# Performance work log

Measured on AMD Instinct MI355X. Metric: run time of the kernel, lower is better.

Reference implementation:

```python
import jax, jax.numpy as jnp
import numpy as np

B, N, DIM, H = 16, 1024, 512, 8
HEAD_DIM = DIM // H
SCALE = HEAD_DIM ** -0.5


def _dct_matrix(m):
    # Orthonormal DCT-II matrix, matching cv2.dct: D[0,:]=sqrt(1/m),
    # D[k,n]=sqrt(2/m)*cos(pi*(2n+1)*k/(2m)) for k>0.
    n = jnp.arange(m, dtype=jnp.float32)
    k = n[:, None]
    D = jnp.sqrt(2.0 / m) * jnp.cos(jnp.pi * (2.0 * n[None, :] + 1.0) * k / (2.0 * m))
    return D.at[0, :].set(jnp.sqrt(1.0 / m))


def setup_inputs() -> dict:
    key = jax.random.key(0)
    ks = jax.random.split(key, 9)
    def lin(k, fan_in, shape):
        return jax.random.normal(k, shape, jnp.float32) * (1.0 / np.sqrt(fan_in))
    return {
        "x": jax.random.normal(ks[0], (B, N, DIM), jnp.float32),
        "qkv_w": lin(ks[1], DIM, (DIM, 3 * DIM)),
        "qkv_b": lin(ks[2], DIM, (3 * DIM,)),
        "proj_w": lin(ks[3], DIM, (DIM, DIM)),
        "proj_b": lin(ks[4], DIM, (DIM,)),
        "h1_w": lin(ks[5], DIM, (DIM, DIM // 4)),
        "h1_b": jnp.zeros((DIM // 4,), jnp.float32),
        "h2_w": lin(ks[6], DIM // 4, (DIM // 4, H)),
        "h2_b": jnp.zeros((H,), jnp.float32),
        "freq_w": jnp.float32(0.5),
    }


def _extract_dct_features(x):
    # x: (B, N, C). Mirrors extract_dct_features incl. the .detach() in torch.
    B_, N_, _ = x.shape
    m = int(np.ceil(np.sqrt(N_)))  # static
    x_mean = x.mean(axis=-1)                                   # (B, N)
    A = jnp.pad(x_mean, ((0, 0), (0, m * m - N_))).reshape(B_, m, m)
    D = _dct_matrix(m)
    dct2 = jnp.einsum('km,bmn,ln->bkl', D, A, D)               # 2D DCT per sample
    dct_feat = dct2.reshape(B_, m * m)[:, :N_]
    dct_feat = jnp.clip(dct_feat, -10.0, 10.0)
    norm = jnp.linalg.norm(dct_feat, axis=1, keepdims=True) + 1e-5
    return jax.lax.stop_gradient(dct_feat / norm)              # (B, N)


def reference(x, qkv_w, qkv_b, proj_w, proj_b, h1_w, h1_b, h2_w, h2_b, freq_w):
    B_, N_, C = x.shape
    # QKV projection -> (3, B, H, N, head_dim)
    qkv = (x @ qkv_w + qkv_b).reshape(B_, N_, 3, H, C // H)
    qkv = jnp.transpose(qkv, (2, 0, 3, 1, 4))
    q, k, v = qkv[0] * SCALE, qkv[1], qkv[2]
    attn = jnp.einsum('bhnd,bhmd->bhnm', q, k)                 # (B, H, N, N)

    # Frequency-domain attention term
    dct_feat = _extract_dct_features(x)                        # (B, N)
    x_avg = x.mean(axis=1)                                     # (B, C)
    head_w = jax.nn.relu(x_avg @ h1_w + h1_b) @ h2_w + h2_b    # (B, H)
    weighted = dct_feat[:, None, :] * head_w[:, :, None]       # (B, H, N)
    freq_attn = jnp.einsum('bhn,bhm->bnm', weighted, weighted) # (B, N, N)
    row_sum = jnp.maximum(freq_attn.sum(axis=-1, keepdims=True), 1e-5)
    freq_attn = jnp.clip(freq_attn / row_sum, 0.0, 1.0)

    aw = jax.nn.sigmoid(freq_w)
    attn = (1.0 - aw) * attn + aw * freq_attn[:, None, :, :]
    attn = jax.nn.softmax(attn, axis=-1)

    out = jnp.einsum('bhnm,bhmd->bhnd', attn, v)
    out = jnp.transpose(out, (0, 2, 1, 3)).reshape(B_, N_, C)
    return out @ proj_w + proj_b
```

## Files before the change

### kernel.cpp

```cpp
#include <hip/hip_runtime.h>
#include <hip/hip_bf16.h>
#include <math.h>

#define PI_F  3.14159265358979323846f
#define LOG2E 1.44269504088896340736f

typedef __attribute__((ext_vector_type(8))) short          bf16x8;
typedef __attribute__((ext_vector_type(8))) unsigned short ushort8;
typedef __attribute__((ext_vector_type(4))) float          f32x4;

__device__ __forceinline__ unsigned short f2bf(float f) {
  union { float f; unsigned u; } v; v.f = f;
  unsigned r = v.u + 0x7fffu + ((v.u >> 16) & 1u);
  return (unsigned short)(r >> 16);
}

__device__ __forceinline__ unsigned short f2bf_hw(float f) {
  __hip_bfloat16 h = __float2bfloat16(f);
  return *reinterpret_cast<unsigned short*>(&h);
}

#define GLOAD16(g, l)                                                         \
  __builtin_amdgcn_global_load_lds(                                           \
      (const __attribute__((address_space(1))) void*)(g),                     \
      (__attribute__((address_space(3))) void*)(l), 16, 0, 0)

static const size_t OFF_XB  = 0;
static const size_t OFF_QB  = 16777216;
static const size_t OFF_KB  = 33554432;
static const size_t OFF_VT  = 67108864;
static const size_t OFF_AO  = 83886080;
static const size_t OFF_WT  = 100663296;
static const size_t OFF_PWT = 102236160;
static const size_t OFF_XM  = 102760448;
static const size_t OFF_XA  = 102825984;
static const size_t OFF_DF  = 102858752;
static const size_t OFF_TS  = 102924288;
static const size_t OFF_CR  = 102924352;

__global__ __launch_bounds__(256) void k_xmean_cvt(const float* __restrict__ x,
                                                   float* __restrict__ xmean,
                                                   unsigned short* __restrict__ xb) {
  int row  = blockIdx.x * 4 + (threadIdx.x >> 6);
  int lane = threadIdx.x & 63;
  const float* px = x + (size_t)row * 512 + lane * 8;
  float4 a = ((const float4*)px)[0];
  float4 b = ((const float4*)px)[1];
  ushort8 o;
  o[0] = f2bf(a.x); o[1] = f2bf(a.y); o[2] = f2bf(a.z); o[3] = f2bf(a.w);
  o[4] = f2bf(b.x); o[5] = f2bf(b.y); o[6] = f2bf(b.z); o[7] = f2bf(b.w);
  *(ushort8*)(xb + (size_t)row * 512 + lane * 8) = o;
  float s = a.x + a.y + a.z + a.w + b.x + b.y + b.z + b.w;
  for (int off = 32; off; off >>= 1) s += __shfl_down(s, off);
  if (lane == 0) xmean[row] = s * (1.f / 512.f);
}

__global__ __launch_bounds__(512) void k_xavg(const unsigned short* __restrict__ xb,
                                              float* __restrict__ xavg) {
  int b = blockIdx.x, chunk = blockIdx.y;
  int c = threadIdx.x;
  const unsigned short* px = xb + ((size_t)b * 1024 + (size_t)chunk * 64) * 512 + c;
  float s = 0.f;
#pragma unroll 8
  for (int n = 0; n < 64; ++n) {
    unsigned u = (unsigned)px[(size_t)n * 512] << 16;
    s += *reinterpret_cast<float*>(&u);
  }
  atomicAdd(&xavg[b * 512 + c], s);
}

__global__ __launch_bounds__(1024) void k_dct(const float* __restrict__ xmean,
                                              float* __restrict__ dfeat,
                                              float* __restrict__ tsum) {
  __shared__ float A[32][33], Dm[32][33], Tm[32][33];
  __shared__ float red[1024];
  __shared__ float nrm;
  int b = blockIdx.x, t = threadIdx.x;
  int kk = t >> 5, nn = t & 31;
  A[kk][nn] = xmean[b * 1024 + t];
  float dv = (kk == 0) ? sqrtf(1.f / 32.f)
                       : sqrtf(2.f / 32.f) * cosf(PI_F * (2.f * nn + 1.f) * (float)kk / 64.f);
  Dm[kk][nn] = dv;
  __syncthreads();
  float acc = 0.f;
  for (int m = 0; m < 32; ++m) acc += Dm[kk][m] * A[m][nn];
  Tm[kk][nn] = acc;
  __syncthreads();
  float acc2 = 0.f;
  for (int n = 0; n < 32; ++n) acc2 += Tm[kk][n] * Dm[nn][n];
  float val = fminf(fmaxf(acc2, -10.f), 10.f);
  red[t] = val * val;
  __syncthreads();
  for (int s = 512; s; s >>= 1) { if (t < s) red[t] += red[t + s]; __syncthreads(); }
  if (t == 0) nrm = sqrtf(red[0]) + 1e-5f;
  __syncthreads();
  float dn = val / nrm;
  dfeat[b * 1024 + t] = dn;
  red[t] = dn;
  __syncthreads();
  for (int s = 512; s; s >>= 1) { if (t < s) red[t] += red[t + s]; __syncthreads(); }
  if (t == 0) tsum[b] = red[0];
}

__global__ __launch_bounds__(128) void k_headw(const float* __restrict__ xavg,
                                               const float* __restrict__ h1w,
                                               const float* __restrict__ h1b,
                                               const float* __restrict__ h2w,
                                               const float* __restrict__ h2b,
                                               const float* __restrict__ dfeat,
                                               const float* __restrict__ tsum,
                                               const float* __restrict__ freqw,
                                               float* __restrict__ crow) {
  __shared__ float xa[512];
  __shared__ float h1s[128];
  __shared__ float hw[8];
  int b = blockIdx.x, t = threadIdx.x;
  for (int i = t; i < 512; i += 128) xa[i] = xavg[b * 512 + i] * (1.f / 1024.f);
  __syncthreads();
  float acc = h1b[t];
  for (int c = 0; c < 512; ++c) acc += xa[c] * h1w[c * 128 + t];
  h1s[t] = fmaxf(acc, 0.f);
  __syncthreads();
  if (t < 8) {
    float a2 = h2b[t];
    for (int j = 0; j < 128; ++j) a2 += h1s[j] * h2w[j * 8 + t];
    hw[t] = a2;
  }
  __syncthreads();
  float s = 0.f;
#pragma unroll
  for (int h = 0; h < 8; ++h) s += hw[h] * hw[h];
  float Tb = tsum[b];
  const float aw2 = (1.f / (1.f + __expf(-freqw[0]))) * LOG2E;
  for (int n = t; n < 1024; n += 128) {
    float dn = dfeat[b * 1024 + n];
    float p = s * dn;
    crow[b * 1024 + n] = aw2 * p / fmaxf(p * Tb, 1e-5f);
  }
}

__global__ __launch_bounds__(256) void k_wtrans(const float* __restrict__ w,
                                                unsigned short* __restrict__ wt,
                                                int Nw) {
  __shared__ unsigned short T[64 * 65];
  int n0 = blockIdx.x * 64, k0 = blockIdx.y * 64;
  int t = threadIdx.x;
  int r = t >> 2, c0 = (t & 3) * 16;
  const float* src = w + (size_t)(k0 + r) * Nw + n0 + c0;
#pragma unroll
  for (int q = 0; q < 4; ++q) {
    float4 v4 = *(const float4*)(src + q * 4);
    T[(c0 + q * 4 + 0) * 65 + r] = f2bf(v4.x);
    T[(c0 + q * 4 + 1) * 65 + r] = f2bf(v4.y);
    T[(c0 + q * 4 + 2) * 65 + r] = f2bf(v4.z);
    T[(c0 + q * 4 + 3) * 65 + r] = f2bf(v4.w);
  }
  __syncthreads();
  int nl = t >> 2, koff = (t & 3) * 16;
  ushort8 o0, o1;
#pragma unroll
  for (int e = 0; e < 8; ++e) o0[e] = T[nl * 65 + koff + e];
#pragma unroll
  for (int e = 0; e < 8; ++e) o1[e] = T[nl * 65 + koff + 8 + e];
  unsigned short* dst = wt + (size_t)(n0 + nl) * 512 + k0 + koff;
  *(ushort8*)(dst) = o0;
  *(ushort8*)(dst + 8) = o1;
}

template <int MODE>
__global__ __launch_bounds__(256) void k_gemm(const unsigned short* __restrict__ A,
                                              const unsigned short* __restrict__ Bt,
                                              const float* __restrict__ bias,
                                              const float* __restrict__ freqw,
                                              unsigned short* __restrict__ o_q,
                                              unsigned short* __restrict__ o_k,
                                              unsigned short* __restrict__ o_vt,
                                              float* __restrict__ o_f) {
  __shared__ __align__(16) unsigned short As[128 * 64];
  __shared__ __align__(16) unsigned short Bs[128 * 64];
  const int t = threadIdx.x, w = t >> 6, l = t & 63;
  const int lg = l >> 4, ln = l & 15;
  const int wm = w >> 1, wn = w & 1;
  constexpr int NX = (MODE == 0) ? 12 : 4;
  const int bid = blockIdx.x, xcd = bid & 7, idx = bid >> 3;
  const int bx = idx % NX, by = xcd * 16 + idx / NX;
  const int row0 = by * 128, col0 = bx * 128;

  f32x4 acc[4][4];
#pragma unroll
  for (int i = 0; i < 4; ++i)
#pragma unroll
    for (int j = 0; j < 4; ++j) acc[i][j] = (f32x4){0.f, 0.f, 0.f, 0.f};

  int aoff[4][2], boff[4][2];
#pragma unroll
  for (int mt = 0; mt < 4; ++mt)
#pragma unroll
    for (int ks = 0; ks < 2; ++ks) {
      int ra = wm * 64 + mt * 16 + ln;
      aoff[mt][ks] = ra * 64 + (((lg + ks * 4) ^ (ra & 7)) << 3);
      int rb = wn * 64 + mt * 16 + ln;
      boff[mt][ks] = rb * 64 + (((lg + ks * 4) ^ (rb & 7)) << 3);
    }

  for (int k0 = 0; k0 < 512; k0 += 64) {
#pragma unroll
    for (int j = 0; j < 4; ++j) {
      int g = (j * 4 + w) * 64 + l;
      int row = g >> 3, slot = g & 7;
      int ss = slot ^ (row & 7);
      GLOAD16(A + (size_t)(row0 + row) * 512 + k0 + ss * 8, As + (size_t)(j * 4 + w) * 512);
      GLOAD16(Bt + (size_t)(col0 + row) * 512 + k0 + ss * 8, Bs + (size_t)(j * 4 + w) * 512);
    }
    __syncthreads();
#pragma unroll
    for (int ks = 0; ks < 2; ++ks) {
      bf16x8 av[4], bv[4];
#pragma unroll
      for (int mt = 0; mt < 4; ++mt) av[mt] = *(const bf16x8*)(As + aoff[mt][ks]);
#pragma unroll
      for (int nt = 0; nt < 4; ++nt) bv[nt] = *(const bf16x8*)(Bs + boff[nt][ks]);
#pragma unroll
      for (int mt = 0; mt < 4; ++mt)
#pragma unroll
        for (int nt = 0; nt < 4; ++nt)
          acc[mt][nt] = __builtin_amdgcn_mfma_f32_16x16x32_bf16(av[mt], bv[nt], acc[mt][nt], 0, 0, 0);
    }
    __syncthreads();
  }

  if (MODE == 0) {
    const int sel = col0 >> 9;
    if (sel == 2) {
      unsigned short* T = (wn == 0) ? As : Bs;
#pragma unroll
      for (int nt = 0; nt < 4; ++nt) {
        int dcol = nt * 16 + ln;
        float bcol = bias[col0 + wn * 64 + dcol];
#pragma unroll
        for (int mt = 0; mt < 4; ++mt)
#pragma unroll
          for (int r = 0; r < 4; ++r) {
            int rowL = wm * 64 + mt * 16 + lg * 4 + r;
            int slot = (rowL >> 3) ^ (dcol & 7);
            T[dcol * 128 + slot * 8 + (rowL & 7)] = f2bf(acc[mt][nt][r] + bcol);
          }
      }
      __syncthreads();
      int b_ = row0 >> 10, n0 = row0 & 1023;
      int h0 = (col0 & 511) >> 6;
      int dcol = t >> 2, rseg = (t & 3) * 32;
#pragma unroll
      for (int half = 0; half < 2; ++half) {
        const unsigned short* S = half ? Bs : As;
        size_t plane = ((size_t)(b_ * 8 + h0 + half)) << 16;
        unsigned short* dst = o_vt + plane + (size_t)dcol * 1024 + n0 + rseg;
#pragma unroll
        for (int j = 0; j < 4; ++j) {
          int slot = ((rseg >> 3) + j) ^ (dcol & 7);
          *(ushort8*)(dst + j * 8) = *(const ushort8*)(S + dcol * 128 + slot * 8);
        }
      }
      return;
    }
    unsigned short* outp = (sel == 0) ? o_q : o_k;
    const float aw = 1.f / (1.f + __expf(-freqw[0]));
    const float scl = (sel == 0) ? 0.125f * (1.f - aw) * LOG2E : 1.f;
#pragma unroll
    for (int nt = 0; nt < 4; ++nt) {
      int colg = col0 + wn * 64 + nt * 16 + ln;
      float bcol = bias[colg];
      int h = (colg >> 6) & 7, d = colg & 63;
#pragma unroll
      for (int mt = 0; mt < 4; ++mt)
#pragma unroll
        for (int r = 0; r < 4; ++r) {
          int row = row0 + wm * 64 + mt * 16 + lg * 4 + r;
          int bidx = row >> 10, n = row & 1023;
          float val = (acc[mt][nt][r] + bcol) * scl;
          outp[(((size_t)(bidx * 8 + h)) << 16) + (n << 6) + d] = f2bf(val);
        }
    }
  } else {
#pragma unroll
    for (int nt = 0; nt < 4; ++nt) {
      int colg = col0 + wn * 64 + nt * 16 + ln;
      float bcol = bias[colg];
#pragma unroll
      for (int mt = 0; mt < 4; ++mt)
#pragma unroll
        for (int r = 0; r < 4; ++r) {
          int row = row0 + wm * 64 + mt * 16 + lg * 4 + r;
          o_f[(size_t)row * 512 + colg] = acc[mt][nt][r] + bcol;
        }
    }
  }
}

__global__ __launch_bounds__(256) void k_attn(const unsigned short* __restrict__ qb,
                                              const unsigned short* __restrict__ kb,
                                              const unsigned short* __restrict__ vtg,
                                              const float* __restrict__ crow,
                                              const float* __restrict__ dfeat,
                                              const float* __restrict__ freqw,
                                              unsigned short* __restrict__ ao) {
  __shared__ __align__(16) unsigned short Ks[64 * 64];
  __shared__ __align__(16) unsigned short Vs[64 * 64];
  __shared__ __align__(16) unsigned short Ps[4][32 * 64];
  const int bid = blockIdx.x, xcd = bid & 7, idx = bid >> 3;
  const int bh = xcd * 16 + (idx >> 3), qt = idx & 7;
  const int b = bh >> 3, h = bh & 7;
  const int t = threadIdx.x, w = t >> 6, l = t & 63;
  const int lg = l >> 4, ln = l & 15;
  const size_t base = ((size_t)(b * 8 + h)) << 16;
  const float aw2 = (1.f / (1.f + __expf(-freqw[0]))) * LOG2E;

  const int qrow0 = qt * 128 + w * 32;
  bf16x8 qf[2][2];
#pragma unroll
  for (int mt = 0; mt < 2; ++mt)
#pragma unroll
    for (int ks = 0; ks < 2; ++ks)
      qf[mt][ks] = *(const bf16x8*)(qb + base + (size_t)(qrow0 + mt * 16 + ln) * 64 + lg * 8 + ks * 32);

  float cr2[2][4];
#pragma unroll
  for (int mt = 0; mt < 2; ++mt)
#pragma unroll
    for (int r = 0; r < 4; ++r)
      cr2[mt][r] = crow[b * 1024 + qrow0 + mt * 16 + lg * 4 + r];

  f32x4 accO[2][4];
#pragma unroll
  for (int mt = 0; mt < 2; ++mt)
#pragma unroll
    for (int dt = 0; dt < 4; ++dt) accO[mt][dt] = (f32x4){0.f, 0.f, 0.f, 0.f};
  float mrow[2][4], psum[2][4];
#pragma unroll
  for (int mt = 0; mt < 2; ++mt)
#pragma unroll
    for (int r = 0; r < 4; ++r) { mrow[mt][r] = -1e30f; psum[mt][r] = 0.f; }

  int rdoff[2];
#pragma unroll
  for (int ks = 0; ks < 2; ++ks) rdoff[ks] = ln * 64 + (((lg + ks * 4) ^ (ln & 7)) << 3);
  int pwoff[4][4];
#pragma unroll
  for (int nt = 0; nt < 4; ++nt)
#pragma unroll
    for (int r = 0; r < 4; ++r) {
      int prow = lg * 4 + r;
      pwoff[nt][r] = prow * 64 + ((((nt << 1) | (ln >> 3)) ^ (prow & 7)) << 3) + (ln & 7);
    }

  for (int kt = 0; kt < 16; ++kt) {
    __syncthreads();
#pragma unroll
    for (int j = 0; j < 2; ++j) {
      int g = (j * 4 + w) * 64 + l;
      int row = g >> 3, slot = g & 7;
      int ss = slot ^ (row & 7);
      GLOAD16(kb + base + (size_t)(kt * 64 + row) * 64 + ss * 8, Ks + (size_t)(j * 4 + w) * 512);
      GLOAD16(vtg + base + (size_t)row * 1024 + kt * 64 + ss * 8, Vs + (size_t)(j * 4 + w) * 512);
    }
    __syncthreads();

    float dmv[4];
#pragma unroll
    for (int nt = 0; nt < 4; ++nt) dmv[nt] = dfeat[b * 1024 + kt * 64 + nt * 16 + ln];
    f32x4 s[2][4];
#pragma unroll
    for (int mt = 0; mt < 2; ++mt)
#pragma unroll
      for (int nt = 0; nt < 4; ++nt)
#pragma unroll
        for (int r = 0; r < 4; ++r)
          s[mt][nt][r] = fminf(fmaxf(cr2[mt][r] * dmv[nt], 0.f), aw2);
#pragma unroll
    for (int nt = 0; nt < 4; ++nt) {
      bf16x8 kf0 = *(const bf16x8*)(Ks + nt * 1024 + rdoff[0]);
      bf16x8 kf1 = *(const bf16x8*)(Ks + nt * 1024 + rdoff[1]);
#pragma unroll
      for (int mt = 0; mt < 2; ++mt) {
        s[mt][nt] = __builtin_amdgcn_mfma_f32_16x16x32_bf16(qf[mt][0], kf0, s[mt][nt], 0, 0, 0);
        s[mt][nt] = __builtin_amdgcn_mfma_f32_16x16x32_bf16(qf[mt][1], kf1, s[mt][nt], 0, 0, 0);
      }
    }

    float lmax[2][4];
    bool viol = false;
#pragma unroll
    for (int mt = 0; mt < 2; ++mt)
#pragma unroll
      for (int r = 0; r < 4; ++r) {
        lmax[mt][r] = fmaxf(fmaxf(s[mt][0][r], s[mt][1][r]), fmaxf(s[mt][2][r], s[mt][3][r]));
        viol = viol || (lmax[mt][r] > mrow[mt][r] + 8.f);
      }
    if (__any(viol)) {
#pragma unroll
      for (int mt = 0; mt < 2; ++mt)
#pragma unroll
        for (int r = 0; r < 4; ++r) {
          float pmax = lmax[mt][r];
          pmax = fmaxf(pmax, __shfl_xor(pmax, 1));
          pmax = fmaxf(pmax, __shfl_xor(pmax, 2));
          pmax = fmaxf(pmax, __shfl_xor(pmax, 4));
          pmax = fmaxf(pmax, __shfl_xor(pmax, 8));
          float mnew = fmaxf(mrow[mt][r], pmax);
          float sc = exp2f(mrow[mt][r] - mnew);
          psum[mt][r] *= sc;
          mrow[mt][r] = mnew;
#pragma unroll
          for (int dt = 0; dt < 4; ++dt) accO[mt][dt][r] *= sc;
        }
    }
#pragma unroll
    for (int mt = 0; mt < 2; ++mt)
#pragma unroll
      for (int r = 0; r < 4; ++r) {
        float p0 = exp2f(s[mt][0][r] - mrow[mt][r]);
        float p1 = exp2f(s[mt][1][r] - mrow[mt][r]);
        float p2 = exp2f(s[mt][2][r] - mrow[mt][r]);
        float p3 = exp2f(s[mt][3][r] - mrow[mt][r]);
        psum[mt][r] += (p0 + p1) + (p2 + p3);
        Ps[w][mt * 1024 + pwoff[0][r]] = f2bf_hw(p0);
        Ps[w][mt * 1024 + pwoff[1][r]] = f2bf_hw(p1);
        Ps[w][mt * 1024 + pwoff[2][r]] = f2bf_hw(p2);
        Ps[w][mt * 1024 + pwoff[3][r]] = f2bf_hw(p3);
      }

    bf16x8 pa[2][2];
#pragma unroll
    for (int mt = 0; mt < 2; ++mt)
#pragma unroll
      for (int ks = 0; ks < 2; ++ks)
        pa[mt][ks] = *(const bf16x8*)(Ps[w] + mt * 1024 + rdoff[ks]);
#pragma unroll
    for (int dt = 0; dt < 4; ++dt) {
      bf16x8 vf0 = *(const bf16x8*)(Vs + dt * 1024 + rdoff[0]);
      bf16x8 vf1 = *(const bf16x8*)(Vs + dt * 1024 + rdoff[1]);
#pragma unroll
      for (int mt = 0; mt < 2; ++mt) {
        accO[mt][dt] = __builtin_amdgcn_mfma_f32_16x16x32_bf16(pa[mt][0], vf0, accO[mt][dt], 0, 0, 0);
        accO[mt][dt] = __builtin_amdgcn_mfma_f32_16x16x32_bf16(pa[mt][1], vf1, accO[mt][dt], 0, 0, 0);
      }
    }
  }

#pragma unroll
  for (int mt = 0; mt < 2; ++mt)
#pragma unroll
    for (int r = 0; r < 4; ++r) {
      float lr = psum[mt][r];
      lr += __shfl_xor(lr, 1);
      lr += __shfl_xor(lr, 2);
      lr += __shfl_xor(lr, 4);
      lr += __shfl_xor(lr, 8);
      float inv = 1.f / lr;
      int n = qrow0 + mt * 16 + lg * 4 + r;
#pragma unroll
      for (int dt = 0; dt < 4; ++dt)
        ao[((size_t)(b * 1024 + n)) * 512 + h * 64 + dt * 16 + ln] = f2bf(accO[mt][dt][r] * inv);
    }
}

extern "C" void kernel_launch(void* const* d_in, const int* in_sizes, int n_in,
                              void* d_out, int out_size, void* d_ws, size_t ws_size,
                              hipStream_t stream) {
  const float* x      = (const float*)d_in[0];
  const float* qkv_w  = (const float*)d_in[1];
  const float* qkv_b  = (const float*)d_in[2];
  const float* proj_w = (const float*)d_in[3];
  const float* proj_b = (const float*)d_in[4];
  const float* h1_w   = (const float*)d_in[5];
  const float* h1_b   = (const float*)d_in[6];
  const float* h2_w   = (const float*)d_in[7];
  const float* h2_b   = (const float*)d_in[8];
  const float* freq_w = (const float*)d_in[9];

  char* ws = (char*)d_ws;
  unsigned short* xb  = (unsigned short*)(ws + OFF_XB);
  unsigned short* qbp = (unsigned short*)(ws + OFF_QB);
  unsigned short* kbp = (unsigned short*)(ws + OFF_KB);
  unsigned short* vtg = (unsigned short*)(ws + OFF_VT);
  unsigned short* ao  = (unsigned short*)(ws + OFF_AO);
  unsigned short* wt  = (unsigned short*)(ws + OFF_WT);
  unsigned short* pwt = (unsigned short*)(ws + OFF_PWT);
  float* xmean = (float*)(ws + OFF_XM);
  float* xavg  = (float*)(ws + OFF_XA);
  float* dfeat = (float*)(ws + OFF_DF);
  float* tsum  = (float*)(ws + OFF_TS);
  float* crow  = (float*)(ws + OFF_CR);
  float* out   = (float*)d_out;

  hipMemsetAsync(xavg, 0, 16 * 512 * sizeof(float), stream);

  k_xmean_cvt<<<dim3(4096), 256, 0, stream>>>(x, xmean, xb);
  k_xavg<<<dim3(16, 16), 512, 0, stream>>>(xb, xavg);
  k_dct<<<dim3(16), 1024, 0, stream>>>(xmean, dfeat, tsum);
  k_headw<<<dim3(16), 128, 0, stream>>>(xavg, h1_w, h1_b, h2_w, h2_b, dfeat, tsum, freq_w, crow);
  k_wtrans<<<dim3(24, 8), 256, 0, stream>>>(qkv_w, wt, 1536);
  k_wtrans<<<dim3(8, 8), 256, 0, stream>>>(proj_w, pwt, 512);
  k_gemm<0><<<dim3(12 * 128), 256, 0, stream>>>(xb, wt, qkv_b, freq_w, qbp, kbp, vtg, nullptr);
  k_attn<<<dim3(1024), 256, 0, stream>>>(qbp, kbp, vtg, crow, dfeat, freq_w, ao);
  k_gemm<1><<<dim3(4 * 128), 256, 0, stream>>>(ao, pwt, proj_b, freq_w, nullptr, nullptr, nullptr, out);
}
```

Baseline: 204.3 us.

## Double-buffer K/V tiles in attention kernel with prefetch of next tile

The attention kernel now keeps two LDS buffers for the K and V tiles. It issues the asynchronous global-to-LDS loads for tile kt+1 while computing on tile kt, which also cuts the per-iteration barriers from two to one. The goal is to hide global load latency behind the QK and PV MFMA work. In exchange, LDS use per block grows by 16 KB, which may lower the number of resident blocks per CU.

```diff
diff --git a/kernel.cpp b/kernel.cpp
--- a/kernel.cpp
+++ b/kernel.cpp
@@ -304,8 +304,8 @@
                                               const float* __restrict__ dfeat,
                                               const float* __restrict__ freqw,
                                               unsigned short* __restrict__ ao) {
-  __shared__ __align__(16) unsigned short Ks[64 * 64];
-  __shared__ __align__(16) unsigned short Vs[64 * 64];
+  __shared__ __align__(16) unsigned short Ks[2][64 * 64];
+  __shared__ __align__(16) unsigned short Vs[2][64 * 64];
   __shared__ __align__(16) unsigned short Ps[4][32 * 64];
   const int bid = blockIdx.x, xcd = bid & 7, idx = bid >> 3;
   const int bh = xcd * 16 + (idx >> 3), qt = idx & 7;
@@ -315,6 +315,10 @@
   const size_t base = ((size_t)(b * 8 + h)) << 16;
   const float aw2 = (1.f / (1.f + __expf(-freqw[0]))) * LOG2E;
 
+  const int g0 = w * 64 + l, g1 = (4 + w) * 64 + l;
+  const int srow0 = g0 >> 3, sslot0 = (g0 & 7) ^ (srow0 & 7);
+  const int srow1 = g1 >> 3, sslot1 = (g1 & 7) ^ (srow1 & 7);
+
   const int qrow0 = qt * 128 + w * 32;
   bf16x8 qf[2][2];
 #pragma unroll
@@ -353,17 +357,21 @@
       pwoff[nt][r] = prow * 64 + ((((nt << 1) | (ln >> 3)) ^ (prow & 7)) << 3) + (ln & 7);
     }
 
+  GLOAD16(kb + base + (size_t)srow0 * 64 + sslot0 * 8, Ks[0] + (size_t)w * 512);
+  GLOAD16(vtg + base + (size_t)srow0 * 1024 + sslot0 * 8, Vs[0] + (size_t)w * 512);
+  GLOAD16(kb + base + (size_t)srow1 * 64 + sslot1 * 8, Ks[0] + (size_t)(4 + w) * 512);
+  GLOAD16(vtg + base + (size_t)srow1 * 1024 + sslot1 * 8, Vs[0] + (size_t)(4 + w) * 512);
+
   for (int kt = 0; kt < 16; ++kt) {
+    const int cur = kt & 1;
     __syncthreads();
-#pragma unroll
-    for (int j = 0; j < 2; ++j) {
-      int g = (j * 4 + w) * 64 + l;
-      int row = g >> 3, slot = g & 7;
-      int ss = slot ^ (row & 7);
-      GLOAD16(kb + base + (size_t)(kt * 64 + row) * 64 + ss * 8, Ks + (size_t)(j * 4 + w) * 512);
-      GLOAD16(vtg + base + (size_t)row * 1024 + kt * 64 + ss * 8, Vs + (size_t)(j * 4 + w) * 512);
-    }
-    __syncthreads();
+    if (kt < 15) {
+      const int kn = kt + 1;
+      GLOAD16(kb + base + (size_t)(kn * 64 + srow0) * 64 + sslot0 * 8, Ks[cur ^ 1] + (size_t)w * 512);
+      GLOAD16(vtg + base + (size_t)srow0 * 1024 + kn * 64 + sslot0 * 8, Vs[cur ^ 1] + (size_t)w * 512);
+      GLOAD16(kb + base + (size_t)(kn * 64 + srow1) * 64 + sslot1 * 8, Ks[cur ^ 1] + (size_t)(4 + w) * 512);
+      GLOAD16(vtg + base + (size_t)srow1 * 1024 + kn * 64 + sslot1 * 8, Vs[cur ^ 1] + (size_t)(4 + w) * 512);
+    }
 
     float dmv[4];
 #pragma unroll
@@ -378,8 +386,8 @@
           s[mt][nt][r] = fminf(fmaxf(cr2[mt][r] * dmv[nt], 0.f), aw2);
 #pragma unroll
     for (int nt = 0; nt < 4; ++nt) {
-      bf16x8 kf0 = *(const bf16x8*)(Ks + nt * 1024 + rdoff[0]);
-      bf16x8 kf1 = *(const bf16x8*)(Ks + nt * 1024 + rdoff[1]);
+      bf16x8 kf0 = *(const bf16x8*)(Ks[cur] + nt * 1024 + rdoff[0]);
+      bf16x8 kf1 = *(const bf16x8*)(Ks[cur] + nt * 1024 + rdoff[1]);
 #pragma unroll
       for (int mt = 0; mt < 2; ++mt) {
         s[mt][nt] = __builtin_amdgcn_mfma_f32_16x16x32_bf16(qf[mt][0], kf0, s[mt][nt], 0, 0, 0);
@@ -437,8 +445,8 @@
         pa[mt][ks] = *(const bf16x8*)(Ps[w] + mt * 1024 + rdoff[ks]);
 #pragma unroll
     for (int dt = 0; dt < 4; ++dt) {
-      bf16x8 vf0 = *(const bf16x8*)(Vs + dt * 1024 + rdoff[0]);
-      bf16x8 vf1 = *(const bf16x8*)(Vs + dt * 1024 + rdoff[1]);
+      bf16x8 vf0 = *(const bf16x8*)(Vs[cur] + dt * 1024 + rdoff[0]);
+      bf16x8 vf1 = *(const bf16x8*)(Vs[cur] + dt * 1024 + rdoff[1]);
 #pragma unroll
       for (int mt = 0; mt < 2; ++mt) {
         accO[mt][dt] = __builtin_amdgcn_mfma_f32_16x16x32_bf16(pa[mt][0], vf0, accO[mt][dt], 0, 0, 0);
```

After: 203.5 us. Within noise of the previous version (-0.4%).
